# Kernel optimization log

Measured on AMD Instinct MI355X. Metric: run time of the kernel, lower is better.

Reference implementation:

```python
import jax, jax.numpy as jnp
import numpy as np

B, S, E, H = 2, 2048, 1024, 16
HD = E // H

def setup_inputs() -> dict:
    key = jax.random.key(0)
    ks = jax.random.split(key, 12)
    q = jax.random.normal(ks[0], (B, S, E), jnp.float32)
    k = jax.random.normal(ks[1], (B, S, E), jnp.float32)
    v = jax.random.normal(ks[2], (B, S, E), jnp.float32)
    # causal mask: 1.0 where attention is disallowed (upper triangle)
    mask = jnp.triu(jnp.ones((S, S), jnp.float32), k=1)[None, None, :, :]
    w = lambda kk: jax.random.normal(kk, (E, E), jnp.float32) * 0.02
    return {
        "q": q, "k": k, "v": v, "mask": mask,
        "Wq": w(ks[3]), "bq": jnp.zeros((E,), jnp.float32),
        "Wk": w(ks[4]), "bk": jnp.zeros((E,), jnp.float32),
        "Wv": w(ks[5]), "bv": jnp.zeros((E,), jnp.float32),
        "Wz": w(ks[6]), "bz": jnp.zeros((E,), jnp.float32),
    }

def _create_heads(x):
    # Faithful to tf.reshape(tf.transpose(x), (B, H, -1, HD)):
    # tf.transpose reverses all dims: [B,S,E] -> [E,S,B], then reshape.
    return jnp.transpose(x, (2, 1, 0)).reshape(B, H, -1, HD)

def reference(q, k, v, mask, Wq, bq, Wk, bk, Wv, bv, Wz, bz):
    qh = _create_heads(q @ Wq + bq)  # (B,H,S,HD)
    kh = _create_heads(k @ Wk + bk)
    vh = _create_heads(v @ Wv + bv)
    qn = qh / jnp.linalg.norm(qh, axis=-1, keepdims=True)
    kn = kh / jnp.linalg.norm(kh, axis=-1, keepdims=True)
    logits = jnp.einsum('bhqd,bhkd->bhqk', qn, kn) * 1000.0
    logits = logits + mask * -1000000000.0
    attn = jax.nn.softmax(logits, axis=-1)  # (B,H,S,S)
    z = jnp.einsum('bhqk,bhkd->bhqd', attn, vh)
    zc = jnp.transpose(z, (0, 2, 1, 3)).reshape(B, -1, E)
    return zc @ Wz + bz, attn
```

## Files before the change

kernel.cpp:

```cpp
#include <hip/hip_runtime.h>
#include <cstdint>
#include <cstddef>


typedef __bf16 bf16x4 __attribute__((ext_vector_type(4)));
typedef __bf16 bf16x8 __attribute__((ext_vector_type(8)));
typedef float floatx4 __attribute__((ext_vector_type(4)));

#define GLOAD_LDS16(g, l)                                                      \
    __builtin_amdgcn_global_load_lds(                                          \
        (const __attribute__((address_space(1))) void*)(g),                    \
        (__attribute__((address_space(3))) void*)(l), 16, 0, 0)

__global__ __launch_bounds__(256) void split_a(
    const float* __restrict__ x0, const float* __restrict__ x1,
    const float* __restrict__ x2, __bf16* __restrict__ ApBase)
{
    const float* X = blockIdx.z == 0 ? x0 : (blockIdx.z == 1 ? x1 : x2);
    __bf16* Ap = ApBase + (size_t)blockIdx.z * (4096ull * 2048);
    const int idx = blockIdx.x * 256 + threadIdx.x;
    const int r = idx >> 8;
    const int c = (idx & 255) * 4;
    float4 t = *(const float4*)(X + (size_t)r * 1024 + c);
    bf16x4 hi, lo;
    hi[0] = (__bf16)t.x; lo[0] = (__bf16)(t.x - (float)hi[0]);
    hi[1] = (__bf16)t.y; lo[1] = (__bf16)(t.y - (float)hi[1]);
    hi[2] = (__bf16)t.z; lo[2] = (__bf16)(t.z - (float)hi[2]);
    hi[3] = (__bf16)t.w; lo[3] = (__bf16)(t.w - (float)hi[3]);
    *(bf16x4*)(Ap + (size_t)r * 2048 + c) = hi;
    *(bf16x4*)(Ap + (size_t)r * 2048 + 1024 + c) = lo;
}

__global__ __launch_bounds__(256) void split_bt(
    const float* __restrict__ w0, const float* __restrict__ w1,
    const float* __restrict__ w2, __bf16* __restrict__ dstBase, size_t dstStride)
{
    const float* W = blockIdx.z == 0 ? w0 : (blockIdx.z == 1 ? w1 : w2);
    __bf16* Bp = dstBase + (size_t)blockIdx.z * dstStride;
    __shared__ float tile[64][65];
    const int tid = (int)threadIdx.x;
    const int k0 = blockIdx.y * 64, n0 = blockIdx.x * 64;
    #pragma unroll
    for (int p = 0; p < 4; ++p) {
        int kr = p * 16 + (tid >> 4);
        float4 t = *(const float4*)(W + (size_t)(k0 + kr) * 1024 + n0 + (tid & 15) * 4);
        tile[kr][(tid & 15) * 4 + 0] = t.x; tile[kr][(tid & 15) * 4 + 1] = t.y;
        tile[kr][(tid & 15) * 4 + 2] = t.z; tile[kr][(tid & 15) * 4 + 3] = t.w;
    }
    __syncthreads();
    const int nr = tid >> 2, kc = (tid & 3) * 16;
    bf16x8 hi0, hi1, lo0, lo1;
    #pragma unroll
    for (int j = 0; j < 8; ++j) {
        float x = tile[kc + j][nr];
        __bf16 h = (__bf16)x; hi0[j] = h; lo0[j] = (__bf16)(x - (float)h);
        float y = tile[kc + 8 + j][nr];
        __bf16 g = (__bf16)y; hi1[j] = g; lo1[j] = (__bf16)(y - (float)g);
    }
    __bf16* row = Bp + (size_t)(n0 + nr) * 2048;
    *(bf16x8*)(row + k0 + kc)          = hi0;
    *(bf16x8*)(row + k0 + kc + 8)      = hi1;
    *(bf16x8*)(row + 1024 + k0 + kc)     = lo0;
    *(bf16x8*)(row + 1024 + k0 + kc + 8) = lo1;
}

__global__ __launch_bounds__(256) void gemm_split(
    const __bf16* __restrict__ Ap0, const __bf16* __restrict__ Bp0,
    const float* __restrict__ b0, const float* __restrict__ b1,
    const float* __restrict__ b2, float* __restrict__ Out0,
    int transposeOut)
{
    const int z = blockIdx.z;
    const __bf16* Ap = Ap0 + (size_t)z * (4096ull * 2048);
    const __bf16* Bp = Bp0 + (size_t)z * (1024ull * 2048);
    const float* bias = z == 0 ? b0 : (z == 1 ? b1 : b2);
    float* Out = Out0 + (size_t)z * (4096ull * 1024);

    __shared__ __bf16 As[128 * 32];
    __shared__ __bf16 Bs[128 * 32];

    const int tid = (int)threadIdx.x;
    const int wave = tid >> 6, lane = tid & 63;
    const int quad = lane >> 4, tl = lane & 15;
    const int m0 = blockIdx.y * 128, n0 = blockIdx.x * 128;
    const int waveM = wave >> 1, waveN = wave & 1;

    floatx4 acc[4][4];
    #pragma unroll
    for (int i = 0; i < 4; ++i)
        #pragma unroll
        for (int j = 0; j < 4; ++j)
            acc[i][j] = (floatx4){0.f, 0.f, 0.f, 0.f};

    const int sRow  = (wave << 4) + (lane >> 2);
    const int sColB = (lane & 3) << 4;
    auto* AsL = (__attribute__((address_space(3))) char*)As;
    auto* BsL = (__attribute__((address_space(3))) char*)Bs;
    const int ldsOff = wave * 1024;

    const int aOffs[3] = {0, 1024, 0};
    const int bOffs[3] = {0, 0, 1024};

    for (int ch = 0; ch < 3; ++ch) {
        const __bf16* Ach = Ap + aOffs[ch];
        const __bf16* Bch = Bp + bOffs[ch];
        for (int k0 = 0; k0 < 1024; k0 += 32) {
            __syncthreads();
            #pragma unroll
            for (int i = 0; i < 2; ++i) {
                GLOAD_LDS16(
                    (const char*)(Ach + (size_t)(m0 + i * 64 + sRow) * 2048 + k0) + sColB,
                    AsL + i * 4096 + ldsOff);
                GLOAD_LDS16(
                    (const char*)(Bch + (size_t)(n0 + i * 64 + sRow) * 2048 + k0) + sColB,
                    BsL + i * 4096 + ldsOff);
            }
            __syncthreads();

            bf16x8 af[4], bfr[4];
            #pragma unroll
            for (int mt = 0; mt < 4; ++mt)
                af[mt] = *(const bf16x8*)(As + (waveM * 64 + mt * 16 + tl) * 32 + quad * 8);
            #pragma unroll
            for (int nt = 0; nt < 4; ++nt)
                bfr[nt] = *(const bf16x8*)(Bs + (waveN * 64 + nt * 16 + tl) * 32 + quad * 8);
            #pragma unroll
            for (int mt = 0; mt < 4; ++mt)
                #pragma unroll
                for (int nt = 0; nt < 4; ++nt)
                    acc[mt][nt] = __builtin_amdgcn_mfma_f32_16x16x32_bf16(
                        af[mt], bfr[nt], acc[mt][nt], 0, 0, 0);
        }
    }

    if (transposeOut) {
        #pragma unroll
        for (int nt = 0; nt < 4; ++nt) {
            const int e = n0 + waveN * 64 + nt * 16 + tl;
            const float bb = bias[e];
            #pragma unroll
            for (int mt = 0; mt < 4; ++mt) {
                floatx4 v = acc[mt][nt] + bb;
                *(floatx4*)(Out + (size_t)e * 4096 + m0 + waveM * 64 + mt * 16 + quad * 4) = v;
            }
        }
    } else {
        #pragma unroll
        for (int mt = 0; mt < 4; ++mt) {
            const int rbase = m0 + waveM * 64 + mt * 16 + quad * 4;
            #pragma unroll
            for (int nt = 0; nt < 4; ++nt) {
                const int e = n0 + waveN * 64 + nt * 16 + tl;
                const float bb = bias[e];
                #pragma unroll
                for (int reg = 0; reg < 4; ++reg)
                    Out[(size_t)(rbase + reg) * 1024 + e] = acc[mt][nt][reg] + bb;
            }
        }
    }
}

__global__ __launch_bounds__(256) void gather_qk(
    const float* __restrict__ PT, __bf16* __restrict__ Outp)
{
    const int tid  = (int)threadIdx.x;
    const int lane = tid & 63;
    const int vec  = blockIdx.x * 4 + (tid >> 6);
    const int head = vec >> 11;
    const int sp   = vec & 2047;
    const int c    = (head >> 4) * 512 + (head & 15) * 32 + (sp >> 6);
    const int src  = (lane & 1) * 2048 + (sp & 63) * 32 + (lane >> 1);
    float v = PT[(size_t)c * 4096 + src];
    float ss = v * v;
    #pragma unroll
    for (int mk = 32; mk >= 1; mk >>= 1) ss += __shfl_xor(ss, mk);
    v = v / sqrtf(ss);
    __bf16 h = (__bf16)v;
    Outp[(size_t)vec * 128 + lane]      = h;
    Outp[(size_t)vec * 128 + 64 + lane] = (__bf16)(v - (float)h);
}

__global__ __launch_bounds__(256) void v_transpose(
    const float* __restrict__ PTv, __bf16* __restrict__ Vt)
{
    const int head = blockIdx.y, st = blockIdx.x;
    const int tid = (int)threadIdx.x;
    const int c = (head >> 4) * 512 + (head & 15) * 32 + st;
    const float* __restrict__ row = PTv + (size_t)c * 4096;

    __shared__ float tile[64][65];
    #pragma unroll
    for (int i = 0; i < 4; ++i) {
        int o = i * 1024 + tid * 4;
        float4 t = *(const float4*)(row + o);
        float vals[4] = {t.x, t.y, t.z, t.w};
        #pragma unroll
        for (int e = 0; e < 4; ++e) {
            int oo = o + e;
            int d  = ((oo & 2047) & 31) * 2 + (oo >> 11);
            int sl = (oo & 2047) >> 5;
            tile[sl][d] = vals[e];
        }
    }
    __syncthreads();

    const int d = tid >> 2, jb = (tid & 3) * 16;
    bf16x8 h0, h1, l0, l1;
    #pragma unroll
    for (int j = 0; j < 8; ++j) {
        float x = tile[jb + j][d];
        __bf16 hh = (__bf16)x; h0[j] = hh; l0[j] = (__bf16)(x - (float)hh);
        float y = tile[jb + 8 + j][d];
        __bf16 gg = (__bf16)y; h1[j] = gg; l1[j] = (__bf16)(y - (float)gg);
    }
    size_t bh = ((size_t)head * 128 + d) * 2048 + st * 64 + jb;
    size_t bl = ((size_t)head * 128 + 64 + d) * 2048 + st * 64 + jb;
    *(bf16x8*)(Vt + bh)     = h0;
    *(bf16x8*)(Vt + bh + 8) = h1;
    *(bf16x8*)(Vt + bl)     = l0;
    *(bf16x8*)(Vt + bl + 8) = l1;
}

__global__ __launch_bounds__(256) void attn_mfma(
    const __bf16* __restrict__ Qp, const __bf16* __restrict__ Kp,
    const __bf16* __restrict__ Vt, float* __restrict__ Attn,
    __bf16* __restrict__ Az)
{
    const int flat = (int)blockIdx.x;
    const int head = flat & 31;
    const int it   = 31 - (flat >> 5);
    const int tid = (int)threadIdx.x;
    const int w = tid >> 6, lane = tid & 63;
    const int quad = lane >> 4, tl = lane & 15;
    const int t7 = tl & 7;
    const int i0 = it * 64;

    const __bf16* __restrict__ Qh = Qp + ((size_t)head * 2048 + i0) * 128;
    const __bf16* __restrict__ Kh = Kp + (size_t)head * 2048 * 128;
    const __bf16* __restrict__ Vh = Vt + (size_t)head * 128 * 2048;
    float* __restrict__ Ah = Attn + (size_t)head * ((size_t)2048 * 2048);

    __shared__ __bf16 kb[64 * 128];
    __shared__ __bf16 vt[128 * 64];
    __shared__ __bf16 ps[4][16 * 72];
    __bf16* psw = ps[w];
    auto* kbL = (__attribute__((address_space(3))) char*)kb;
    auto* vtL = (__attribute__((address_space(3))) char*)vt;

    const char* kSrc[4];
    const char* vSrc[4];
    #pragma unroll
    for (int i = 0; i < 4; ++i) {
        int d  = w * 256 + i * 64 + lane;
        int rK = d >> 4, cK = (d & 15) ^ (rK & 7);
        kSrc[i] = (const char*)(Kh + (size_t)rK * 128) + cK * 16;
        int rV = d >> 3, cV = (d & 7) ^ (rV & 7);
        vSrc[i] = (const char*)(Vh + (size_t)rV * 2048) + cV * 16;
    }
    const int ok0 = ((quad)      ^ t7) * 8;
    const int ok1 = ((quad + 4)  ^ t7) * 8;
    const int ok2 = ((quad + 8)  ^ t7) * 8;
    const int ok3 = ((quad + 12) ^ t7) * 8;

    const __bf16* qrow = Qh + (size_t)(w * 16 + tl) * 128;
    bf16x8 qhi0 = *(const bf16x8*)(qrow + quad * 8);
    bf16x8 qhi1 = *(const bf16x8*)(qrow + 32 + quad * 8);
    bf16x8 qlo0 = *(const bf16x8*)(qrow + 64 + quad * 8);
    bf16x8 qlo1 = *(const bf16x8*)(qrow + 96 + quad * 8);

    for (int jt = it + 1; jt < 32; ++jt) {
        float4 z4 = make_float4(0.f, 0.f, 0.f, 0.f);
        #pragma unroll
        for (int g = 0; g < 4; ++g)
            *(float4*)(Ah + (size_t)(i0 + w * 16 + g * 4 + quad) * 2048
                          + jt * 64 + tl * 4) = z4;
    }

    float m[4], l[4];
    #pragma unroll
    for (int r = 0; r < 4; ++r) { m[r] = -3.0e38f; l[r] = 0.0f; }

    for (int jt = 0; jt <= it; ++jt) {
        __syncthreads();
        #pragma unroll
        for (int i = 0; i < 4; ++i)
            GLOAD_LDS16(kSrc[i] + (size_t)jt * 16384, kbL + w * 4096 + i * 1024);
        __syncthreads();

        floatx4 S[4];
        #pragma unroll
        for (int sub = 0; sub < 4; ++sub) {
            const __bf16* kr = kb + (sub * 16 + tl) * 128;
            bf16x8 khi0 = *(const bf16x8*)(kr + ok0);
            bf16x8 khi1 = *(const bf16x8*)(kr + ok1);
            bf16x8 klo0 = *(const bf16x8*)(kr + ok2);
            bf16x8 klo1 = *(const bf16x8*)(kr + ok3);
            floatx4 s = (floatx4){0.f, 0.f, 0.f, 0.f};
            s = __builtin_amdgcn_mfma_f32_16x16x32_bf16(qhi0, khi0, s, 0, 0, 0);
            s = __builtin_amdgcn_mfma_f32_16x16x32_bf16(qhi1, khi1, s, 0, 0, 0);
            s = __builtin_amdgcn_mfma_f32_16x16x32_bf16(qhi0, klo0, s, 0, 0, 0);
            s = __builtin_amdgcn_mfma_f32_16x16x32_bf16(qhi1, klo1, s, 0, 0, 0);
            s = __builtin_amdgcn_mfma_f32_16x16x32_bf16(qlo0, khi0, s, 0, 0, 0);
            s = __builtin_amdgcn_mfma_f32_16x16x32_bf16(qlo1, khi1, s, 0, 0, 0);
            S[sub] = s;
        }
        const bool diag = (jt == it);
        #pragma unroll
        for (int reg = 0; reg < 4; ++reg) {
            const int irow = w * 16 + quad * 4 + reg;
            float sl[4];
            #pragma unroll
            for (int sub = 0; sub < 4; ++sub) {
                float lv = S[sub][reg] * 1000.0f;
                if (diag && (sub * 16 + tl > irow)) lv = -1.0e9f;
                sl[sub] = lv;
            }
            float mt = fmaxf(fmaxf(sl[0], sl[1]), fmaxf(sl[2], sl[3]));
            float mn = fmaxf(m[reg], mt);
            l[reg] = l[reg] * __expf(m[reg] - mn)
                   + __expf(sl[0]-mn) + __expf(sl[1]-mn)
                   + __expf(sl[2]-mn) + __expf(sl[3]-mn);
            m[reg] = mn;
        }
    }

    #pragma unroll
    for (int reg = 0; reg < 4; ++reg) {
        #pragma unroll
        for (int mk = 8; mk >= 1; mk >>= 1) {
            float mo = __shfl_xor(m[reg], mk);
            float lo = __shfl_xor(l[reg], mk);
            float mn = fmaxf(m[reg], mo);
            l[reg] = l[reg] * __expf(m[reg] - mn) + lo * __expf(mo - mn);
            m[reg] = mn;
        }
    }
    float inv_l[4];
    #pragma unroll
    for (int reg = 0; reg < 4; ++reg) inv_l[reg] = 1.0f / l[reg];

    floatx4 zacc[4];
    #pragma unroll
    for (int t = 0; t < 4; ++t) zacc[t] = (floatx4){0.f, 0.f, 0.f, 0.f};

    for (int jt = 0; jt <= it; ++jt) {
        __syncthreads();
        #pragma unroll
        for (int i = 0; i < 4; ++i) {
            GLOAD_LDS16(kSrc[i] + (size_t)jt * 16384, kbL + w * 4096 + i * 1024);
            GLOAD_LDS16(vSrc[i] + (size_t)jt * 128,   vtL + w * 4096 + i * 1024);
        }
        __syncthreads();

        floatx4 S[4];
        #pragma unroll
        for (int sub = 0; sub < 4; ++sub) {
            const __bf16* kr = kb + (sub * 16 + tl) * 128;
            bf16x8 khi0 = *(const bf16x8*)(kr + ok0);
            bf16x8 khi1 = *(const bf16x8*)(kr + ok1);
            bf16x8 klo0 = *(const bf16x8*)(kr + ok2);
            bf16x8 klo1 = *(const bf16x8*)(kr + ok3);
            floatx4 s = (floatx4){0.f, 0.f, 0.f, 0.f};
            s = __builtin_amdgcn_mfma_f32_16x16x32_bf16(qhi0, khi0, s, 0, 0, 0);
            s = __builtin_amdgcn_mfma_f32_16x16x32_bf16(qhi1, khi1, s, 0, 0, 0);
            s = __builtin_amdgcn_mfma_f32_16x16x32_bf16(qhi0, klo0, s, 0, 0, 0);
            s = __builtin_amdgcn_mfma_f32_16x16x32_bf16(qhi1, klo1, s, 0, 0, 0);
            s = __builtin_amdgcn_mfma_f32_16x16x32_bf16(qlo0, khi0, s, 0, 0, 0);
            s = __builtin_amdgcn_mfma_f32_16x16x32_bf16(qlo1, khi1, s, 0, 0, 0);
            S[sub] = s;
        }
        const bool diag = (jt == it);
        #pragma unroll
        for (int reg = 0; reg < 4; ++reg) {
            const int irow = w * 16 + quad * 4 + reg;
            #pragma unroll
            for (int sub = 0; sub < 4; ++sub) {
                float lv = S[sub][reg] * 1000.0f;
                if (diag && (sub * 16 + tl > irow)) lv = -1.0e9f;
                float p = __expf(lv - m[reg]) * inv_l[reg];
                psw[(quad * 4 + reg) * 72 + sub * 16 + tl] = (__bf16)p;
            }
        }
        __asm__ volatile("s_waitcnt lgkmcnt(0)" ::: "memory");

        #pragma unroll
        for (int g = 0; g < 4; ++g) {
            bf16x4 pv = *(const bf16x4*)(psw + (g * 4 + quad) * 72 + tl * 4);
            float4 f = make_float4((float)pv[0], (float)pv[1],
                                   (float)pv[2], (float)pv[3]);
            *(float4*)(Ah + (size_t)(i0 + w * 16 + g * 4 + quad) * 2048
                          + jt * 64 + tl * 4) = f;
        }

        bf16x8 p0 = *(const bf16x8*)(psw + tl * 72 + quad * 8);
        bf16x8 p1 = *(const bf16x8*)(psw + tl * 72 + 32 + quad * 8);

        #pragma unroll
        for (int t = 0; t < 4; ++t) {
            const __bf16* vh0 = vt + (t * 16 + tl) * 64;
            const __bf16* vl0 = vt + (64 + t * 16 + tl) * 64;
            bf16x8 vhi0 = *(const bf16x8*)(vh0 + ok0);
            bf16x8 vhi1 = *(const bf16x8*)(vh0 + ok1);
            bf16x8 vlo0 = *(const bf16x8*)(vl0 + ok0);
            bf16x8 vlo1 = *(const bf16x8*)(vl0 + ok1);
            zacc[t] = __builtin_amdgcn_mfma_f32_16x16x32_bf16(p0, vhi0, zacc[t], 0, 0, 0);
            zacc[t] = __builtin_amdgcn_mfma_f32_16x16x32_bf16(p1, vhi1, zacc[t], 0, 0, 0);
            zacc[t] = __builtin_amdgcn_mfma_f32_16x16x32_bf16(p0, vlo0, zacc[t], 0, 0, 0);
            zacc[t] = __builtin_amdgcn_mfma_f32_16x16x32_bf16(p1, vlo1, zacc[t], 0, 0, 0);
        }
    }

    const int b = head >> 4, h = head & 15;
    #pragma unroll
    for (int reg = 0; reg < 4; ++reg) {
        const size_t R = (size_t)b * 2048 + i0 + w * 16 + quad * 4 + reg;
        #pragma unroll
        for (int t = 0; t < 4; ++t) {
            float x = zacc[t][reg];
            __bf16 hh = (__bf16)x;
            Az[R * 2048 + h * 64 + t * 16 + tl]        = hh;
            Az[R * 2048 + 1024 + h * 64 + t * 16 + tl] = (__bf16)(x - (float)hh);
        }
    }
}

extern "C" void kernel_launch(void* const* d_in, const int* in_sizes, int n_in,
                              void* d_out, int out_size, void* d_ws, size_t ws_size,
                              hipStream_t stream) {
    (void)in_sizes; (void)n_in; (void)out_size;
    const float* q  = (const float*)d_in[0];
    const float* k  = (const float*)d_in[1];
    const float* v  = (const float*)d_in[2];
    const float* Wq = (const float*)d_in[4];  const float* bq = (const float*)d_in[5];
    const float* Wk = (const float*)d_in[6];  const float* bk = (const float*)d_in[7];
    const float* Wv = (const float*)d_in[8];  const float* bv = (const float*)d_in[9];
    const float* Wz = (const float*)d_in[10]; const float* bz = (const float*)d_in[11];

    float* out0 = (float*)d_out;
    float* attn = out0 + 4194304;

    float*  PT0 = attn;
    __bf16* Ap0 = (__bf16*)(attn + 12582912);
    __bf16* Bp0 = (__bf16*)(attn + 12582912 + 12582912);

    __bf16* Bpz = (__bf16*)d_in[4];

    __bf16 *Qp, *Kp, *Vtp, *Az;
    if (ws_size >= (size_t)67108864) {
        __bf16* ws = (__bf16*)d_ws;
        Qp = ws; Kp = ws + 8388608; Vtp = ws + 16777216; Az = ws + 25165824;
    } else {
        Qp = (__bf16*)d_in[0]; Kp = (__bf16*)d_in[1]; Vtp = (__bf16*)d_in[2];
        Az = (__bf16*)d_ws;
    }

    split_a <<<dim3(4096, 1, 3), 256, 0, stream>>>(q, k, v, Ap0);
    split_bt<<<dim3(16, 16, 3), 256, 0, stream>>>(Wq, Wk, Wv, Bp0, 1024ull*2048);

    gemm_split<<<dim3(8, 32, 3), 256, 0, stream>>>(Ap0, Bp0, bq, bk, bv, PT0, 1);

    gather_qk  <<<16384, 256, 0, stream>>>(PT0,           Qp);
    gather_qk  <<<16384, 256, 0, stream>>>(PT0 + 4194304, Kp);
    v_transpose<<<dim3(32, 32), 256, 0, stream>>>(PT0 + 8388608, Vtp);

    split_bt<<<dim3(16, 16, 1), 256, 0, stream>>>(Wz, Wz, Wz, Bpz, 0);

    attn_mfma<<<dim3(1024), 256, 0, stream>>>(Qp, Kp, Vtp, attn, Az);

    gemm_split<<<dim3(8, 32, 1), 256, 0, stream>>>(Az, Bpz, bz, bz, bz, out0, 0);
}
```

Baseline: 967.9 us.

## Merge split-bf16 GEMM chunks into one K loop and enlarge attention query tile

The split-precision GEMM now loads the hi and lo parts of A and B together in each K step and issues three MFMA passes, where before it ran three separate K passes. This cuts barrier and loop overhead and reuses the hi fragments. The attention kernel moves to 512-thread blocks covering 128 query rows, so each K/V tile load is shared by 8 waves instead of 4. Waves whose rows are entirely above a tile skip its compute and write zeros. This doubles LDS reuse but adds causal imbalance inside a block, and the 512-thread launch bound may constrain registers.

```diff
diff --git a/kernel.cpp b/kernel.cpp
--- a/kernel.cpp
+++ b/kernel.cpp
@@ -76,8 +76,8 @@
     const float* bias = z == 0 ? b0 : (z == 1 ? b1 : b2);
     float* Out = Out0 + (size_t)z * (4096ull * 1024);
 
-    __shared__ __bf16 As[128 * 32];
-    __shared__ __bf16 Bs[128 * 32];
+    __shared__ __bf16 As[2 * 128 * 32];
+    __shared__ __bf16 Bs[2 * 128 * 32];
 
     const int tid = (int)threadIdx.x;
     const int wave = tid >> 6, lane = tid & 63;
@@ -98,39 +98,52 @@
     auto* BsL = (__attribute__((address_space(3))) char*)Bs;
     const int ldsOff = wave * 1024;
 
-    const int aOffs[3] = {0, 1024, 0};
-    const int bOffs[3] = {0, 0, 1024};
-
-    for (int ch = 0; ch < 3; ++ch) {
-        const __bf16* Ach = Ap + aOffs[ch];
-        const __bf16* Bch = Bp + bOffs[ch];
-        for (int k0 = 0; k0 < 1024; k0 += 32) {
-            __syncthreads();
-            #pragma unroll
-            for (int i = 0; i < 2; ++i) {
-                GLOAD_LDS16(
-                    (const char*)(Ach + (size_t)(m0 + i * 64 + sRow) * 2048 + k0) + sColB,
-                    AsL + i * 4096 + ldsOff);
-                GLOAD_LDS16(
-                    (const char*)(Bch + (size_t)(n0 + i * 64 + sRow) * 2048 + k0) + sColB,
-                    BsL + i * 4096 + ldsOff);
-            }
-            __syncthreads();
-
-            bf16x8 af[4], bfr[4];
-            #pragma unroll
-            for (int mt = 0; mt < 4; ++mt)
-                af[mt] = *(const bf16x8*)(As + (waveM * 64 + mt * 16 + tl) * 32 + quad * 8);
+    for (int k0 = 0; k0 < 1024; k0 += 32) {
+        __syncthreads();
+        #pragma unroll
+        for (int i = 0; i < 2; ++i) {
+            GLOAD_LDS16((const char*)(Ap + (size_t)(m0 + i*64 + sRow) * 2048 + k0) + sColB,
+                        AsL + i * 4096 + ldsOff);
+            GLOAD_LDS16((const char*)(Ap + 1024 + (size_t)(m0 + i*64 + sRow) * 2048 + k0) + sColB,
+                        AsL + 8192 + i * 4096 + ldsOff);
+            GLOAD_LDS16((const char*)(Bp + (size_t)(n0 + i*64 + sRow) * 2048 + k0) + sColB,
+                        BsL + i * 4096 + ldsOff);
+            GLOAD_LDS16((const char*)(Bp + 1024 + (size_t)(n0 + i*64 + sRow) * 2048 + k0) + sColB,
+                        BsL + 8192 + i * 4096 + ldsOff);
+        }
+        __syncthreads();
+
+        bf16x8 ah[4], bh[4], al[4], bl[4];
+        #pragma unroll
+        for (int mt = 0; mt < 4; ++mt)
+            ah[mt] = *(const bf16x8*)(As + (waveM*64 + mt*16 + tl) * 32 + quad * 8);
+        #pragma unroll
+        for (int nt = 0; nt < 4; ++nt)
+            bh[nt] = *(const bf16x8*)(Bs + (waveN*64 + nt*16 + tl) * 32 + quad * 8);
+        #pragma unroll
+        for (int mt = 0; mt < 4; ++mt)
             #pragma unroll
             for (int nt = 0; nt < 4; ++nt)
-                bfr[nt] = *(const bf16x8*)(Bs + (waveN * 64 + nt * 16 + tl) * 32 + quad * 8);
-            #pragma unroll
-            for (int mt = 0; mt < 4; ++mt)
-                #pragma unroll
-                for (int nt = 0; nt < 4; ++nt)
-                    acc[mt][nt] = __builtin_amdgcn_mfma_f32_16x16x32_bf16(
-                        af[mt], bfr[nt], acc[mt][nt], 0, 0, 0);
-        }
+                acc[mt][nt] = __builtin_amdgcn_mfma_f32_16x16x32_bf16(
+                    ah[mt], bh[nt], acc[mt][nt], 0, 0, 0);
+        #pragma unroll
+        for (int mt = 0; mt < 4; ++mt)
+            al[mt] = *(const bf16x8*)(As + 4096 + (waveM*64 + mt*16 + tl) * 32 + quad * 8);
+        #pragma unroll
+        for (int mt = 0; mt < 4; ++mt)
+            #pragma unroll
+            for (int nt = 0; nt < 4; ++nt)
+                acc[mt][nt] = __builtin_amdgcn_mfma_f32_16x16x32_bf16(
+                    al[mt], bh[nt], acc[mt][nt], 0, 0, 0);
+        #pragma unroll
+        for (int nt = 0; nt < 4; ++nt)
+            bl[nt] = *(const bf16x8*)(Bs + 4096 + (waveN*64 + nt*16 + tl) * 32 + quad * 8);
+        #pragma unroll
+        for (int mt = 0; mt < 4; ++mt)
+            #pragma unroll
+            for (int nt = 0; nt < 4; ++nt)
+                acc[mt][nt] = __builtin_amdgcn_mfma_f32_16x16x32_bf16(
+                    ah[mt], bl[nt], acc[mt][nt], 0, 0, 0);
     }
 
     if (transposeOut) {
@@ -221,19 +234,22 @@
     *(bf16x8*)(Vt + bl + 8) = l1;
 }
 
-__global__ __launch_bounds__(256) void attn_mfma(
+__global__ __launch_bounds__(512, 4) void attn_mfma(
     const __bf16* __restrict__ Qp, const __bf16* __restrict__ Kp,
     const __bf16* __restrict__ Vt, float* __restrict__ Attn,
     __bf16* __restrict__ Az)
 {
     const int flat = (int)blockIdx.x;
     const int head = flat & 31;
-    const int it   = 31 - (flat >> 5);
+    const int it   = 15 - (flat >> 5);
     const int tid = (int)threadIdx.x;
     const int w = tid >> 6, lane = tid & 63;
     const int quad = lane >> 4, tl = lane & 15;
     const int t7 = tl & 7;
-    const int i0 = it * 64;
+    const int i0 = it * 128;
+    const int jtmax = 2 * it + 1;
+    const int wrowMax = i0 + w * 16 + 15;
+    const int wdiag   = (i0 + w * 16) >> 6;
 
     const __bf16* __restrict__ Qh = Qp + ((size_t)head * 2048 + i0) * 128;
     const __bf16* __restrict__ Kh = Kp + (size_t)head * 2048 * 128;
@@ -242,16 +258,16 @@
 
     __shared__ __bf16 kb[64 * 128];
     __shared__ __bf16 vt[128 * 64];
-    __shared__ __bf16 ps[4][16 * 72];
+    __shared__ __bf16 ps[8][16 * 72];
     __bf16* psw = ps[w];
     auto* kbL = (__attribute__((address_space(3))) char*)kb;
     auto* vtL = (__attribute__((address_space(3))) char*)vt;
 
-    const char* kSrc[4];
-    const char* vSrc[4];
-    #pragma unroll
-    for (int i = 0; i < 4; ++i) {
-        int d  = w * 256 + i * 64 + lane;
+    const char* kSrc[2];
+    const char* vSrc[2];
+    #pragma unroll
+    for (int i = 0; i < 2; ++i) {
+        int d  = i * 512 + tid;
         int rK = d >> 4, cK = (d & 15) ^ (rK & 7);
         kSrc[i] = (const char*)(Kh + (size_t)rK * 128) + cK * 16;
         int rV = d >> 3, cV = (d & 7) ^ (rV & 7);
@@ -268,7 +284,7 @@
     bf16x8 qlo0 = *(const bf16x8*)(qrow + 64 + quad * 8);
     bf16x8 qlo1 = *(const bf16x8*)(qrow + 96 + quad * 8);
 
-    for (int jt = it + 1; jt < 32; ++jt) {
+    for (int jt = jtmax + 1; jt < 32; ++jt) {
         float4 z4 = make_float4(0.f, 0.f, 0.f, 0.f);
         #pragma unroll
         for (int g = 0; g < 4; ++g)
@@ -280,12 +296,13 @@
     #pragma unroll
     for (int r = 0; r < 4; ++r) { m[r] = -3.0e38f; l[r] = 0.0f; }
 
-    for (int jt = 0; jt <= it; ++jt) {
-        __syncthreads();
-        #pragma unroll
-        for (int i = 0; i < 4; ++i)
-            GLOAD_LDS16(kSrc[i] + (size_t)jt * 16384, kbL + w * 4096 + i * 1024);
-        __syncthreads();
+    for (int jt = 0; jt <= jtmax; ++jt) {
+        __syncthreads();
+        #pragma unroll
+        for (int i = 0; i < 2; ++i)
+            GLOAD_LDS16(kSrc[i] + (size_t)jt * 16384, kbL + i * 8192 + w * 1024);
+        __syncthreads();
+        if (jt * 64 > wrowMax) continue;
 
         floatx4 S[4];
         #pragma unroll
@@ -304,7 +321,7 @@
             s = __builtin_amdgcn_mfma_f32_16x16x32_bf16(qlo1, khi1, s, 0, 0, 0);
             S[sub] = s;
         }
-        const bool diag = (jt == it);
+        const bool diag = (jt == wdiag);
         #pragma unroll
         for (int reg = 0; reg < 4; ++reg) {
             const int irow = w * 16 + quad * 4 + reg;
@@ -312,7 +329,7 @@
             #pragma unroll
             for (int sub = 0; sub < 4; ++sub) {
                 float lv = S[sub][reg] * 1000.0f;
-                if (diag && (sub * 16 + tl > irow)) lv = -1.0e9f;
+                if (diag && (jt * 64 + sub * 16 + tl > i0 + irow)) lv = -1.0e9f;
                 sl[sub] = lv;
             }
             float mt = fmaxf(fmaxf(sl[0], sl[1]), fmaxf(sl[2], sl[3]));
@@ -343,14 +360,23 @@
     #pragma unroll
     for (int t = 0; t < 4; ++t) zacc[t] = (floatx4){0.f, 0.f, 0.f, 0.f};
 
-    for (int jt = 0; jt <= it; ++jt) {
-        __syncthreads();
-        #pragma unroll
-        for (int i = 0; i < 4; ++i) {
-            GLOAD_LDS16(kSrc[i] + (size_t)jt * 16384, kbL + w * 4096 + i * 1024);
-            GLOAD_LDS16(vSrc[i] + (size_t)jt * 128,   vtL + w * 4096 + i * 1024);
-        }
-        __syncthreads();
+    for (int jt = 0; jt <= jtmax; ++jt) {
+        __syncthreads();
+        #pragma unroll
+        for (int i = 0; i < 2; ++i) {
+            GLOAD_LDS16(kSrc[i] + (size_t)jt * 16384, kbL + i * 8192 + w * 1024);
+            GLOAD_LDS16(vSrc[i] + (size_t)jt * 128,   vtL + i * 8192 + w * 1024);
+        }
+        __syncthreads();
+
+        if (jt * 64 > wrowMax) {
+            float4 z4 = make_float4(0.f, 0.f, 0.f, 0.f);
+            #pragma unroll
+            for (int g = 0; g < 4; ++g)
+                *(float4*)(Ah + (size_t)(i0 + w * 16 + g * 4 + quad) * 2048
+                              + jt * 64 + tl * 4) = z4;
+            continue;
+        }
 
         floatx4 S[4];
         #pragma unroll
@@ -369,14 +395,14 @@
             s = __builtin_amdgcn_mfma_f32_16x16x32_bf16(qlo1, khi1, s, 0, 0, 0);
             S[sub] = s;
         }
-        const bool diag = (jt == it);
+        const bool diag = (jt == wdiag);
         #pragma unroll
         for (int reg = 0; reg < 4; ++reg) {
             const int irow = w * 16 + quad * 4 + reg;
             #pragma unroll
             for (int sub = 0; sub < 4; ++sub) {
                 float lv = S[sub][reg] * 1000.0f;
-                if (diag && (sub * 16 + tl > irow)) lv = -1.0e9f;
+                if (diag && (jt * 64 + sub * 16 + tl > i0 + irow)) lv = -1.0e9f;
                 float p = __expf(lv - m[reg]) * inv_l[reg];
                 psw[(quad * 4 + reg) * 72 + sub * 16 + tl] = (__bf16)p;
             }
@@ -465,7 +491,7 @@
 
     split_bt<<<dim3(16, 16, 1), 256, 0, stream>>>(Wz, Wz, Wz, Bpz, 0);
 
-    attn_mfma<<<dim3(1024), 256, 0, stream>>>(Qp, Kp, Vtp, attn, Az);
+    attn_mfma<<<dim3(512), 512, 0, stream>>>(Qp, Kp, Vtp, attn, Az);
 
     gemm_split<<<dim3(8, 32, 1), 256, 0, stream>>>(Az, Bpz, bz, bz, bz, out0, 0);
 }
```

Measured after the change: 889.2 us. -8.1%, faster.
